# Kernel tuning notes

Measured on AMD Instinct MI355X. Metric: run time of the kernel, lower is better.

Reference implementation:

```python
import jax, jax.numpy as jnp
import numpy as np

N_NODES = 50000
N_EDGES = 800000
D = 128        # in_channels == out_channels
EDGE_DIM = 32
EPS = 0.0      # GINEConv default eps


def setup_inputs() -> dict:
    key = jax.random.key(0)
    ks = jax.random.split(key, 12)
    s = lambda d: 1.0 / np.sqrt(d)
    inp = {
        "x": jax.random.normal(ks[0], (N_NODES, D), jnp.float32),
        "edge_index": jax.random.randint(ks[1], (2, N_EDGES), 0, N_NODES, jnp.int64),
        "edge_attr": jax.random.normal(ks[2], (N_EDGES, EDGE_DIM), jnp.float32),
        "importance": jax.random.uniform(ks[3], (N_NODES, 1), jnp.float32),
        # GINEConv edge lin: Linear(edge_dim, in_channels)
        "We": jax.random.uniform(ks[4], (EDGE_DIM, D), jnp.float32, -s(EDGE_DIM), s(EDGE_DIM)),
        "be": jax.random.uniform(ks[5], (D,), jnp.float32, -s(EDGE_DIM), s(EDGE_DIM)),
        # GINEConv nn: Linear(in_channels, out_channels)
        "Wc": jax.random.uniform(ks[6], (D, D), jnp.float32, -s(D), s(D)),
        "bc": jax.random.uniform(ks[7], (D,), jnp.float32, -s(D), s(D)),
        # importance_gate: Linear(out_channels + 1, out_channels)
        "Wg": jax.random.uniform(ks[8], (D + 1, D), jnp.float32, -s(D + 1), s(D + 1)),
        "bg": jax.random.uniform(ks[9], (D,), jnp.float32, -s(D + 1), s(D + 1)),
        # importance_propagation: Linear(out_channels, 1)
        "Wp": jax.random.uniform(ks[10], (D, 1), jnp.float32, -s(D), s(D)),
        "bp": jax.random.uniform(ks[11], (1,), jnp.float32, -s(D), s(D)),
    }
    return inp


def reference(x, edge_index, edge_attr, importance, We, be, Wc, bc, Wg, bg, Wp, bp):
    src, dst = edge_index[0], edge_index[1]
    # GINEConv: messages = relu(x_j + lin(edge_attr)), aggregated by sum at dst
    e = edge_attr @ We + be                      # [E, D]
    msg = jax.nn.relu(x[src] + e)                # [E, D] gather + fused add/relu
    agg = jax.ops.segment_sum(msg, dst, num_segments=N_NODES)  # [N, D] scatter-add
    conv_out = ((1.0 + EPS) * x + agg) @ Wc + bc  # [N, D]
    # importance gating + residual
    gate_in = jnp.concatenate([conv_out, importance], axis=-1)  # [N, D+1]
    gate = jax.nn.sigmoid(gate_in @ Wg + bg)
    out = gate * conv_out + (1.0 - gate) * x
    propagated_importance = out @ Wp + bp        # [N, 1]
    return (out, propagated_importance)
```

## Files before the change

### kernel.cpp

```cpp
#include <hip/hip_runtime.h>

#define NN 50000
#define NE 800000
#define DD 128
#define ED 32
#define NB 196
#define NCH (NE / 16)

typedef short bf16x8 __attribute__((ext_vector_type(8)));
typedef float f32x4  __attribute__((ext_vector_type(4)));

__device__ __forceinline__ float4 ld4(const float* p) {
    return *reinterpret_cast<const float4*>(p);
}
__device__ __forceinline__ short f2bf(float f) {
    unsigned u = __float_as_uint(f);
    u += 0x7fffu + ((u >> 16) & 1u);
    return (short)(u >> 16);
}
__device__ __forceinline__ float bf2f(short h) {
    return __uint_as_float(((unsigned)(unsigned short)h) << 16);
}
__device__ __forceinline__ int sniff64(const int* ei) {
    return ((ei[1] | ei[3] | ei[5] | ei[7]) == 0) ? 1 : 0;
}

__global__ __launch_bounds__(256)
void k_hist(const int* __restrict__ ei, int* __restrict__ counts) {
    const int is64 = sniff64(ei);
    for (int e = blockIdx.x * blockDim.x + threadIdx.x; e < NE;
         e += gridDim.x * blockDim.x) {
        const int dst = ei[(long)(NE + e) << is64];
        atomicAdd(&counts[dst], 1);
    }
}

__global__ __launch_bounds__(256)
void k_bsum(const int* __restrict__ counts, int* __restrict__ bsum) {
    const int i = blockIdx.x * 256 + threadIdx.x;
    int c = (i < NN) ? counts[i] : 0;
#pragma unroll
    for (int off = 32; off; off >>= 1) c += __shfl_xor(c, off, 64);
    __shared__ int ws4[4];
    if ((threadIdx.x & 63) == 0) ws4[threadIdx.x >> 6] = c;
    __syncthreads();
    if (threadIdx.x == 0) bsum[blockIdx.x] = ws4[0] + ws4[1] + ws4[2] + ws4[3];
}

__global__ __launch_bounds__(256)
void k_scanb(const int* __restrict__ bsum, int* __restrict__ bexcl) {
    const int tid = threadIdx.x, lane = tid & 63, w = tid >> 6;
    const int v = (tid < NB) ? bsum[tid] : 0;
    int s = v;
#pragma unroll
    for (int off = 1; off < 64; off <<= 1) {
        const int t = __shfl_up(s, off, 64);
        if (lane >= off) s += t;
    }
    __shared__ int wsum[4], wexcl[4];
    if (lane == 63) wsum[w] = s;
    __syncthreads();
    if (tid == 0) {
        int r = 0;
#pragma unroll
        for (int k = 0; k < 4; ++k) { wexcl[k] = r; r += wsum[k]; }
    }
    __syncthreads();
    if (tid < NB) bexcl[tid] = wexcl[w] + s - v;
}

__global__ __launch_bounds__(256)
void k_rowptr(const int* __restrict__ counts, const int* __restrict__ bexcl,
              int* __restrict__ cursor) {
    const int tid = threadIdx.x, lane = tid & 63, w = tid >> 6;
    const int i = blockIdx.x * 256 + tid;
    const int c = (i < NN) ? counts[i] : 0;
    int s = c;
#pragma unroll
    for (int off = 1; off < 64; off <<= 1) {
        const int t = __shfl_up(s, off, 64);
        if (lane >= off) s += t;
    }
    __shared__ int wsum[4], wexcl[4];
    if (lane == 63) wsum[w] = s;
    __syncthreads();
    if (tid == 0) {
        int r = 0;
#pragma unroll
        for (int k = 0; k < 4; ++k) { wexcl[k] = r; r += wsum[k]; }
    }
    __syncthreads();
    if (i < NN) cursor[i] = bexcl[blockIdx.x] + wexcl[w] + s - c;
}

__global__ __launch_bounds__(256)
void k_scatter(const int* __restrict__ ei, int* __restrict__ cursor,
               int2* __restrict__ sdat, int* __restrict__ edst) {
    const int is64 = sniff64(ei);
    for (int e = blockIdx.x * blockDim.x + threadIdx.x; e < NE;
         e += gridDim.x * blockDim.x) {
        const int src = ei[(long)e << is64];
        const int dst = ei[(long)(NE + e) << is64];
        const int pos = atomicAdd(&cursor[dst], 1);
        sdat[pos] = make_int2(src, e);
        edst[pos] = dst;
    }
}

__global__ __launch_bounds__(256, 4)
void k_aggE(const float* __restrict__ x, const float* __restrict__ ea,
            const float* __restrict__ We, const float* __restrict__ be,
            const int2* __restrict__ sdat, const int* __restrict__ edst,
            float* __restrict__ agg)
{
    const int lane = threadIdx.x & 63;
    const int ncol = lane & 15;
    const int krow = (lane >> 4) << 3;
    const int grp  = lane >> 4;
    const int wid  = (blockIdx.x << 2) | (threadIdx.x >> 6);
    const int nw   = gridDim.x << 2;

    bf16x8 Bf[8];
    float beb[8];
#pragma unroll
    for (int b = 0; b < 8; ++b) {
#pragma unroll
        for (int i = 0; i < 8; ++i)
            Bf[b][i] = f2bf(We[(krow + i) * DD + b * 16 + ncol]);
        beb[b] = be[b * 16 + ncol];
    }

    if (wid >= NCH) return;

    int2 dv   = sdat[wid * 16 + ncol];
    int  dstv = edst[wid * 16 + ncol];

    for (int c = wid; c < NCH; c += nw) {
        const int cn = min(c + nw, NCH - 1);
        const int2 dvn   = sdat[cn * 16 + ncol];
        const int  dstvn = edst[cn * 16 + ncol];

        const float* ear = ea + (size_t)dv.y * ED + krow;
        const float4 r0 = ld4(ear), r1 = ld4(ear + 4);

        const float* xr[4];
#pragma unroll
        for (int r = 0; r < 4; ++r)
            xr[r] = x + (size_t)__shfl(dv.x, (grp << 2) + r, 64) * DD + ncol;
        f32x4 C[8];
#pragma unroll
        for (int b = 0; b < 8; ++b) {
            f32x4 cc;
            cc[0] = xr[0][b * 16]; cc[1] = xr[1][b * 16];
            cc[2] = xr[2][b * 16]; cc[3] = xr[3][b * 16];
            C[b] = cc;
        }

        bf16x8 Af;
        Af[0] = f2bf(r0.x); Af[1] = f2bf(r0.y);
        Af[2] = f2bf(r0.z); Af[3] = f2bf(r0.w);
        Af[4] = f2bf(r1.x); Af[5] = f2bf(r1.y);
        Af[6] = f2bf(r1.z); Af[7] = f2bf(r1.w);

#pragma unroll
        for (int b = 0; b < 8; ++b)
            C[b] = __builtin_amdgcn_mfma_f32_16x16x32_bf16(Af, Bf[b], C[b], 0, 0, 0);

        float t[8][4];
#pragma unroll
        for (int b = 0; b < 8; ++b)
#pragma unroll
            for (int r = 0; r < 4; ++r)
                t[b][r] = fmaxf(C[b][r] + beb[b], 0.0f);

        const int prv = __shfl(dstv, (lane == 0) ? 0 : lane - 1, 64);
        const bool flag = (lane < 16) && ((ncol == 0) || (dstv != prv));
        const unsigned B16 = (unsigned)__ballot(flag) & 0xFFFFu;

        int sid[4];
#pragma unroll
        for (int r = 0; r < 4; ++r) {
            const int m = (grp << 2) + r;
            sid[r] = __popc(B16 & ((2u << m) - 1)) - 1;
        }

        unsigned rem = B16;
        int s = 0;
        while (rem) {
            const int ms = __ffs((int)rem) - 1;
            rem &= rem - 1;
            const int d = __shfl(dstv, ms, 64);
            float red[8];
#pragma unroll
            for (int b = 0; b < 8; ++b) {
                float v = ((sid[0] == s) ? t[b][0] : 0.0f)
                        + ((sid[1] == s) ? t[b][1] : 0.0f)
                        + ((sid[2] == s) ? t[b][2] : 0.0f)
                        + ((sid[3] == s) ? t[b][3] : 0.0f);
                v += __shfl_xor(v, 16, 64);
                v += __shfl_xor(v, 32, 64);
                red[b] = v;
            }
            float v0 = red[0], v1 = red[4];
            v0 = (grp == 1) ? red[1] : v0;
            v0 = (grp == 2) ? red[2] : v0;
            v0 = (grp == 3) ? red[3] : v0;
            v1 = (grp == 1) ? red[5] : v1;
            v1 = (grp == 2) ? red[6] : v1;
            v1 = (grp == 3) ? red[7] : v1;
            float* ar = agg + (size_t)d * DD;
            unsafeAtomicAdd(ar + lane, v0);
            unsafeAtomicAdd(ar + 64 + lane, v1);
            ++s;
        }

        dv = dvn; dstv = dstvn;
    }
}

__global__ __launch_bounds__(256)
void k_conv(const float* __restrict__ x, const float* agg,
            const float* __restrict__ Wc, const float* __restrict__ bc,
            float* conv)
{
    __shared__ short sBh[2048 * 8];
    __shared__ short sBl[2048 * 8];
    for (int idx = threadIdx.x; idx < 2048; idx += 256) {
        const int kk = idx >> 9;
        const int b  = (idx >> 6) & 7;
        const int l  = idx & 63;
        const int row0 = kk * 32 + ((l >> 4) << 3);
        const int col  = b * 16 + (l & 15);
        bf16x8 h8, l8;
#pragma unroll
        for (int j = 0; j < 8; ++j) {
            const float v = Wc[(row0 + j) * DD + col];
            const short h = f2bf(v);
            h8[j] = h;
            l8[j] = f2bf(v - bf2f(h));
        }
        *reinterpret_cast<bf16x8*>(&sBh[idx * 8]) = h8;
        *reinterpret_cast<bf16x8*>(&sBl[idx * 8]) = l8;
    }
    __syncthreads();

    const int lane = threadIdx.x & 63;
    const int ncol = lane & 15;
    const int krow = (lane >> 4) << 3;
    const int grp  = lane >> 4;
    const int wid  = (blockIdx.x << 2) | (threadIdx.x >> 6);
    if (wid >= NN / 16) return;

    float bcb[8];
#pragma unroll
    for (int b = 0; b < 8; ++b) bcb[b] = bc[b * 16 + ncol];

    const int m0 = wid * 16;
    const float* xrow = x   + (size_t)(m0 + ncol) * DD + krow;
    const float* grow = agg + (size_t)(m0 + ncol) * DD + krow;

    f32x4 C[8];
#pragma unroll
    for (int b = 0; b < 8; ++b) {
        f32x4 c = { bcb[b], bcb[b], bcb[b], bcb[b] };
        C[b] = c;
    }

#pragma unroll
    for (int kk = 0; kk < 4; ++kk) {
        const float4 x0 = ld4(xrow + kk * 32), x1 = ld4(xrow + kk * 32 + 4);
        const float4 g0 = ld4(grow + kk * 32), g1 = ld4(grow + kk * 32 + 4);
        const float av[8] = { x0.x + g0.x, x0.y + g0.y, x0.z + g0.z, x0.w + g0.w,
                              x1.x + g1.x, x1.y + g1.y, x1.z + g1.z, x1.w + g1.w };
        bf16x8 Ah, Al;
#pragma unroll
        for (int j = 0; j < 8; ++j) {
            const short h = f2bf(av[j]);
            Ah[j] = h;
            Al[j] = f2bf(av[j] - bf2f(h));
        }
#pragma unroll
        for (int b = 0; b < 8; ++b) {
            const bf16x8 Bh = *reinterpret_cast<const bf16x8*>(&sBh[((kk * 8 + b) * 64 + lane) * 8]);
            const bf16x8 Bl = *reinterpret_cast<const bf16x8*>(&sBl[((kk * 8 + b) * 64 + lane) * 8]);
            C[b] = __builtin_amdgcn_mfma_f32_16x16x32_bf16(Ah, Bh, C[b], 0, 0, 0);
            C[b] = __builtin_amdgcn_mfma_f32_16x16x32_bf16(Al, Bh, C[b], 0, 0, 0);
            C[b] = __builtin_amdgcn_mfma_f32_16x16x32_bf16(Ah, Bl, C[b], 0, 0, 0);
        }
    }

#pragma unroll
    for (int r = 0; r < 4; ++r) {
        float* crow = conv + (size_t)(m0 + (grp << 2) + r) * DD + ncol;
#pragma unroll
        for (int b = 0; b < 8; ++b) crow[b * 16] = C[b][r];
    }
}

__global__ __launch_bounds__(256)
void k_gate(const float* __restrict__ x, const float* conv,
            const float* __restrict__ imp, const float* __restrict__ Wg,
            const float* __restrict__ bg, const float* __restrict__ Wp,
            const float* __restrict__ bp, float* outp, float* __restrict__ prop)
{
    __shared__ short sBh[2048 * 8];
    __shared__ short sBl[2048 * 8];
    for (int idx = threadIdx.x; idx < 2048; idx += 256) {
        const int kk = idx >> 9;
        const int b  = (idx >> 6) & 7;
        const int l  = idx & 63;
        const int row0 = kk * 32 + ((l >> 4) << 3);
        const int col  = b * 16 + (l & 15);
        bf16x8 h8, l8;
#pragma unroll
        for (int j = 0; j < 8; ++j) {
            const float v = Wg[(row0 + j) * DD + col];
            const short h = f2bf(v);
            h8[j] = h;
            l8[j] = f2bf(v - bf2f(h));
        }
        *reinterpret_cast<bf16x8*>(&sBh[idx * 8]) = h8;
        *reinterpret_cast<bf16x8*>(&sBl[idx * 8]) = l8;
    }
    __syncthreads();

    const int lane = threadIdx.x & 63;
    const int ncol = lane & 15;
    const int krow = (lane >> 4) << 3;
    const int grp  = lane >> 4;
    const int wid  = (blockIdx.x << 2) | (threadIdx.x >> 6);
    if (wid >= NN / 16) return;

    float bgb[8], wgi[8], wp8[8];
#pragma unroll
    for (int b = 0; b < 8; ++b) {
        bgb[b] = bg[b * 16 + ncol];
        wgi[b] = Wg[DD * DD + b * 16 + ncol];
        wp8[b] = Wp[b * 16 + ncol];
    }
    const float bps = bp[0];

    const int m0 = wid * 16;

    float cvD[8][4], xvD[8][4], im[4];
#pragma unroll
    for (int r = 0; r < 4; ++r) {
        const int m = m0 + (grp << 2) + r;
        const float* cr = conv + (size_t)m * DD + ncol;
        const float* xr = x    + (size_t)m * DD + ncol;
        im[r] = imp[m];
#pragma unroll
        for (int b = 0; b < 8; ++b) { cvD[b][r] = cr[b * 16]; xvD[b][r] = xr[b * 16]; }
    }

    f32x4 C[8];
#pragma unroll
    for (int b = 0; b < 8; ++b) {
        f32x4 c = { bgb[b], bgb[b], bgb[b], bgb[b] };
        C[b] = c;
    }

    const float* arow = conv + (size_t)(m0 + ncol) * DD + krow;
#pragma unroll
    for (int kk = 0; kk < 4; ++kk) {
        const float4 a0 = ld4(arow + kk * 32);
        const float4 a1 = ld4(arow + kk * 32 + 4);
        const float av[8] = { a0.x, a0.y, a0.z, a0.w, a1.x, a1.y, a1.z, a1.w };
        bf16x8 Ah, Al;
#pragma unroll
        for (int j = 0; j < 8; ++j) {
            const short h = f2bf(av[j]);
            Ah[j] = h;
            Al[j] = f2bf(av[j] - bf2f(h));
        }
#pragma unroll
        for (int b = 0; b < 8; ++b) {
            const bf16x8 Bh = *reinterpret_cast<const bf16x8*>(&sBh[((kk * 8 + b) * 64 + lane) * 8]);
            const bf16x8 Bl = *reinterpret_cast<const bf16x8*>(&sBl[((kk * 8 + b) * 64 + lane) * 8]);
            C[b] = __builtin_amdgcn_mfma_f32_16x16x32_bf16(Ah, Bh, C[b], 0, 0, 0);
            C[b] = __builtin_amdgcn_mfma_f32_16x16x32_bf16(Al, Bh, C[b], 0, 0, 0);
            C[b] = __builtin_amdgcn_mfma_f32_16x16x32_bf16(Ah, Bl, C[b], 0, 0, 0);
        }
    }

    float s[4] = { 0.f, 0.f, 0.f, 0.f };
#pragma unroll
    for (int r = 0; r < 4; ++r) {
        float* orow = outp + (size_t)(m0 + (grp << 2) + r) * DD + ncol;
#pragma unroll
        for (int b = 0; b < 8; ++b) {
            const float a = C[b][r] + im[r] * wgi[b];
            const float g = 1.0f / (1.0f + expf(-a));
            const float o = fmaf(g, cvD[b][r] - xvD[b][r], xvD[b][r]);
            orow[b * 16] = o;
            s[r] += o * wp8[b];
        }
    }
#pragma unroll
    for (int off = 1; off < 16; off <<= 1) {
        s[0] += __shfl_xor(s[0], off, 64);
        s[1] += __shfl_xor(s[1], off, 64);
        s[2] += __shfl_xor(s[2], off, 64);
        s[3] += __shfl_xor(s[3], off, 64);
    }
    if (ncol < 4) {
        const float v = (ncol == 0) ? s[0] : (ncol == 1) ? s[1] : (ncol == 2) ? s[2] : s[3];
        prop[m0 + (grp << 2) + ncol] = v + bps;
    }
}

extern "C" void kernel_launch(void* const* d_in, const int* in_sizes, int n_in,
                              void* d_out, int out_size, void* d_ws, size_t ws_size,
                              hipStream_t stream) {
    const float* x   = (const float*)d_in[0];
    const int*   ei  = (const int*)d_in[1];
    const float* ea  = (const float*)d_in[2];
    const float* imp = (const float*)d_in[3];
    const float* We  = (const float*)d_in[4];
    const float* be  = (const float*)d_in[5];
    const float* Wc  = (const float*)d_in[6];
    const float* bc  = (const float*)d_in[7];
    const float* Wg  = (const float*)d_in[8];
    const float* bg  = (const float*)d_in[9];
    const float* Wp  = (const float*)d_in[10];
    const float* bp  = (const float*)d_in[11];

    float* out  = (float*)d_out;
    float* prop = out + (size_t)NN * DD;
    float* agg  = out;

    int*  counts = (int*)d_ws;
    int*  cursor = (int*)((char*)d_ws + 204800);
    int*  bsum   = (int*)((char*)d_ws + 409600);
    int*  bexcl  = (int*)((char*)d_ws + 413696);
    int2* sdat   = (int2*)((char*)d_ws + 1048576);
    int*  edst   = (int*)((char*)d_ws + 7448576);

    hipMemsetAsync(counts, 0, NN * sizeof(int), stream);
    hipMemsetAsync(agg, 0, (size_t)NN * DD * sizeof(float), stream);
    hipLaunchKernelGGL(k_hist,    dim3(2048), dim3(256), 0, stream, ei, counts);
    hipLaunchKernelGGL(k_bsum,    dim3(NB),   dim3(256), 0, stream, counts, bsum);
    hipLaunchKernelGGL(k_scanb,   dim3(1),    dim3(256), 0, stream, bsum, bexcl);
    hipLaunchKernelGGL(k_rowptr,  dim3(NB),   dim3(256), 0, stream, counts, bexcl, cursor);
    hipLaunchKernelGGL(k_scatter, dim3(2048), dim3(256), 0, stream, ei, cursor, sdat, edst);
    hipLaunchKernelGGL(k_aggE,    dim3(2048), dim3(256), 0, stream,
                       x, ea, We, be, sdat, edst, agg);
    hipLaunchKernelGGL(k_conv,    dim3(782),  dim3(256), 0, stream, x, agg, Wc, bc, out);
    hipLaunchKernelGGL(k_gate,    dim3(782),  dim3(256), 0, stream,
                       x, out, imp, Wg, bg, Wp, bp, out, prop);
}
```

Baseline: 236.4 us.

## Gather bf16 copy of x and switch edge aggregation to 32x32 MFMA tiles

Adds a pre-pass that converts x to bf16 so the per-edge gather of source rows reads half the bytes. The edge kernel now processes 32-edge chunks with 32x32x16 MFMA (one chunk per wave, no persistent loop, larger grid) and replaces the segment reduction with masked FMA sums. This also rounds x to bf16 inside the message sum, which loses precision, and it drops the prefetch of the next chunk's indices. The persistent grid-stride loop that reused the We fragments is removed, so each wave reloads and converts We.

Measured after the change: 221.2 us. -6.5%, faster.

```diff
diff --git a/kernel.cpp b/kernel.cpp
--- a/kernel.cpp
+++ b/kernel.cpp
@@ -5,10 +5,12 @@
 #define DD 128
 #define ED 32
 #define NB 196
-#define NCH (NE / 16)
-
-typedef short bf16x8 __attribute__((ext_vector_type(8)));
-typedef float f32x4  __attribute__((ext_vector_type(4)));
+#define NC32 (NE / 32)
+
+typedef short  bf16x8 __attribute__((ext_vector_type(8)));
+typedef short  s16x8  __attribute__((ext_vector_type(8)));
+typedef float  f32x4  __attribute__((ext_vector_type(4)));
+typedef float  f32x16 __attribute__((ext_vector_type(16)));
 
 __device__ __forceinline__ float4 ld4(const float* p) {
     return *reinterpret_cast<const float4*>(p);
@@ -23,6 +25,17 @@
 }
 __device__ __forceinline__ int sniff64(const int* ei) {
     return ((ei[1] | ei[3] | ei[5] | ei[7]) == 0) ? 1 : 0;
+}
+
+__global__ __launch_bounds__(256)
+void k_xcast(const float* __restrict__ x, unsigned short* __restrict__ xb) {
+    const int t = blockIdx.x * 256 + threadIdx.x;
+    const int base = t * 8;
+    const float4 a = ld4(x + base), b = ld4(x + base + 4);
+    s16x8 o;
+    o[0] = f2bf(a.x); o[1] = f2bf(a.y); o[2] = f2bf(a.z); o[3] = f2bf(a.w);
+    o[4] = f2bf(b.x); o[5] = f2bf(b.y); o[6] = f2bf(b.z); o[7] = f2bf(b.w);
+    *reinterpret_cast<s16x8*>(xb + base) = o;
 }
 
 __global__ __launch_bounds__(256)
@@ -108,113 +121,96 @@
 }
 
 __global__ __launch_bounds__(256, 4)
-void k_aggE(const float* __restrict__ x, const float* __restrict__ ea,
+void k_aggE(const unsigned short* __restrict__ xb, const float* __restrict__ ea,
             const float* __restrict__ We, const float* __restrict__ be,
             const int2* __restrict__ sdat, const int* __restrict__ edst,
             float* __restrict__ agg)
 {
     const int lane = threadIdx.x & 63;
-    const int ncol = lane & 15;
-    const int krow = (lane >> 4) << 3;
-    const int grp  = lane >> 4;
+    const int col  = lane & 31;
+    const int h    = lane >> 5;
     const int wid  = (blockIdx.x << 2) | (threadIdx.x >> 6);
-    const int nw   = gridDim.x << 2;
-
-    bf16x8 Bf[8];
-    float beb[8];
-#pragma unroll
-    for (int b = 0; b < 8; ++b) {
-#pragma unroll
-        for (int i = 0; i < 8; ++i)
-            Bf[b][i] = f2bf(We[(krow + i) * DD + b * 16 + ncol]);
-        beb[b] = be[b * 16 + ncol];
-    }
-
-    if (wid >= NCH) return;
-
-    int2 dv   = sdat[wid * 16 + ncol];
-    int  dstv = edst[wid * 16 + ncol];
-
-    for (int c = wid; c < NCH; c += nw) {
-        const int cn = min(c + nw, NCH - 1);
-        const int2 dvn   = sdat[cn * 16 + ncol];
-        const int  dstvn = edst[cn * 16 + ncol];
-
-        const float* ear = ea + (size_t)dv.y * ED + krow;
-        const float4 r0 = ld4(ear), r1 = ld4(ear + 4);
-
-        const float* xr[4];
-#pragma unroll
-        for (int r = 0; r < 4; ++r)
-            xr[r] = x + (size_t)__shfl(dv.x, (grp << 2) + r, 64) * DD + ncol;
-        f32x4 C[8];
-#pragma unroll
-        for (int b = 0; b < 8; ++b) {
-            f32x4 cc;
-            cc[0] = xr[0][b * 16]; cc[1] = xr[1][b * 16];
-            cc[2] = xr[2][b * 16]; cc[3] = xr[3][b * 16];
-            C[b] = cc;
-        }
-
-        bf16x8 Af;
-        Af[0] = f2bf(r0.x); Af[1] = f2bf(r0.y);
-        Af[2] = f2bf(r0.z); Af[3] = f2bf(r0.w);
-        Af[4] = f2bf(r1.x); Af[5] = f2bf(r1.y);
-        Af[6] = f2bf(r1.z); Af[7] = f2bf(r1.w);
-
-#pragma unroll
-        for (int b = 0; b < 8; ++b)
-            C[b] = __builtin_amdgcn_mfma_f32_16x16x32_bf16(Af, Bf[b], C[b], 0, 0, 0);
-
-        float t[8][4];
-#pragma unroll
-        for (int b = 0; b < 8; ++b)
-#pragma unroll
-            for (int r = 0; r < 4; ++r)
-                t[b][r] = fmaxf(C[b][r] + beb[b], 0.0f);
-
-        const int prv = __shfl(dstv, (lane == 0) ? 0 : lane - 1, 64);
-        const bool flag = (lane < 16) && ((ncol == 0) || (dstv != prv));
-        const unsigned B16 = (unsigned)__ballot(flag) & 0xFFFFu;
-
-        int sid[4];
-#pragma unroll
-        for (int r = 0; r < 4; ++r) {
-            const int m = (grp << 2) + r;
-            sid[r] = __popc(B16 & ((2u << m) - 1)) - 1;
-        }
-
-        unsigned rem = B16;
-        int s = 0;
-        while (rem) {
-            const int ms = __ffs((int)rem) - 1;
-            rem &= rem - 1;
-            const int d = __shfl(dstv, ms, 64);
-            float red[8];
-#pragma unroll
-            for (int b = 0; b < 8; ++b) {
-                float v = ((sid[0] == s) ? t[b][0] : 0.0f)
-                        + ((sid[1] == s) ? t[b][1] : 0.0f)
-                        + ((sid[2] == s) ? t[b][2] : 0.0f)
-                        + ((sid[3] == s) ? t[b][3] : 0.0f);
-                v += __shfl_xor(v, 16, 64);
-                v += __shfl_xor(v, 32, 64);
-                red[b] = v;
-            }
-            float v0 = red[0], v1 = red[4];
-            v0 = (grp == 1) ? red[1] : v0;
-            v0 = (grp == 2) ? red[2] : v0;
-            v0 = (grp == 3) ? red[3] : v0;
-            v1 = (grp == 1) ? red[5] : v1;
-            v1 = (grp == 2) ? red[6] : v1;
-            v1 = (grp == 3) ? red[7] : v1;
-            float* ar = agg + (size_t)d * DD;
-            unsafeAtomicAdd(ar + lane, v0);
-            unsafeAtomicAdd(ar + 64 + lane, v1);
-            ++s;
-        }
-
-        dv = dvn; dstv = dstvn;
+    if (wid >= NC32) return;
+
+    bf16x8 Bf[4][2];
+    float  beb[4];
+#pragma unroll
+    for (int bb = 0; bb < 4; ++bb) {
+#pragma unroll
+        for (int s = 0; s < 2; ++s)
+#pragma unroll
+            for (int i = 0; i < 8; ++i)
+                Bf[bb][s][i] = f2bf(We[(s * 16 + h * 8 + i) * DD + bb * 32 + col]);
+        beb[bb] = be[bb * 32 + col];
+    }
+
+    const int2 dv   = sdat[wid * 32 + col];
+    const int  dstv = edst[wid * 32 + col];
+
+    unsigned off[16];
+#pragma unroll
+    for (int reg = 0; reg < 16; ++reg) {
+        const int E = (reg & 3) + 8 * (reg >> 2) + 4 * h;
+        const int src = __shfl(dv.x, E, 64);
+        off[reg] = (unsigned)src * DD + col;
+    }
+
+    f32x16 C[4];
+#pragma unroll
+    for (int bb = 0; bb < 4; ++bb)
+#pragma unroll
+        for (int reg = 0; reg < 16; ++reg)
+            C[bb][reg] = __uint_as_float((unsigned)xb[off[reg] + bb * 32] << 16);
+
+    const float* ear = ea + (size_t)dv.y * ED + h * 8;
+    const float4 a00 = ld4(ear),      a01 = ld4(ear + 4);
+    const float4 a10 = ld4(ear + 16), a11 = ld4(ear + 20);
+    bf16x8 Af0, Af1;
+    Af0[0] = f2bf(a00.x); Af0[1] = f2bf(a00.y); Af0[2] = f2bf(a00.z); Af0[3] = f2bf(a00.w);
+    Af0[4] = f2bf(a01.x); Af0[5] = f2bf(a01.y); Af0[6] = f2bf(a01.z); Af0[7] = f2bf(a01.w);
+    Af1[0] = f2bf(a10.x); Af1[1] = f2bf(a10.y); Af1[2] = f2bf(a10.z); Af1[3] = f2bf(a10.w);
+    Af1[4] = f2bf(a11.x); Af1[5] = f2bf(a11.y); Af1[6] = f2bf(a11.z); Af1[7] = f2bf(a11.w);
+
+#pragma unroll
+    for (int bb = 0; bb < 4; ++bb) {
+        C[bb] = __builtin_amdgcn_mfma_f32_32x32x16_bf16(Af0, Bf[bb][0], C[bb], 0, 0, 0);
+        C[bb] = __builtin_amdgcn_mfma_f32_32x32x16_bf16(Af1, Bf[bb][1], C[bb], 0, 0, 0);
+    }
+
+#pragma unroll
+    for (int bb = 0; bb < 4; ++bb)
+#pragma unroll
+        for (int reg = 0; reg < 16; ++reg)
+            C[bb][reg] = fmaxf(C[bb][reg] + beb[bb], 0.0f);
+
+    const int  prv  = __shfl(dstv, (col == 0) ? 0 : col - 1, 64);
+    const bool flag = (lane < 32) && ((col == 0) || (dstv != prv));
+    unsigned rem = (unsigned)(__ballot(flag) & 0xFFFFFFFFull);
+
+    while (rem) {
+        const int ms = __ffs((int)rem) - 1;
+        rem &= rem - 1;
+        const int hi = rem ? (__ffs((int)rem) - 1) : 32;
+        const int d  = __shfl(dstv, ms, 64);
+
+        float v0 = 0.f, v1 = 0.f, v2 = 0.f, v3 = 0.f;
+#pragma unroll
+        for (int reg = 0; reg < 16; ++reg) {
+            const int E = (reg & 3) + 8 * (reg >> 2) + 4 * h;
+            const float mk = (E >= ms && E < hi) ? 1.0f : 0.0f;
+            v0 = fmaf(mk, C[0][reg], v0);
+            v1 = fmaf(mk, C[1][reg], v1);
+            v2 = fmaf(mk, C[2][reg], v2);
+            v3 = fmaf(mk, C[3][reg], v3);
+        }
+        v0 += __shfl_xor(v0, 32, 64);
+        v1 += __shfl_xor(v1, 32, 64);
+        v2 += __shfl_xor(v2, 32, 64);
+        v3 += __shfl_xor(v3, 32, 64);
+
+        float* ar = agg + (size_t)d * DD + h * 64 + col;
+        unsafeAtomicAdd(ar,      h ? v2 : v0);
+        unsafeAtomicAdd(ar + 32, h ? v3 : v1);
     }
 }
 
@@ -429,22 +425,24 @@
     float* prop = out + (size_t)NN * DD;
     float* agg  = out;
 
-    int*  counts = (int*)d_ws;
-    int*  cursor = (int*)((char*)d_ws + 204800);
-    int*  bsum   = (int*)((char*)d_ws + 409600);
-    int*  bexcl  = (int*)((char*)d_ws + 413696);
-    int2* sdat   = (int2*)((char*)d_ws + 1048576);
-    int*  edst   = (int*)((char*)d_ws + 7448576);
+    int*            counts = (int*)d_ws;
+    int*            cursor = (int*)((char*)d_ws + 204800);
+    int*            bsum   = (int*)((char*)d_ws + 409600);
+    int*            bexcl  = (int*)((char*)d_ws + 413696);
+    int2*           sdat   = (int2*)((char*)d_ws + 1048576);
+    int*            edst   = (int*)((char*)d_ws + 7448576);
+    unsigned short* xb     = (unsigned short*)((char*)d_ws + 10649600);
 
     hipMemsetAsync(counts, 0, NN * sizeof(int), stream);
     hipMemsetAsync(agg, 0, (size_t)NN * DD * sizeof(float), stream);
+    hipLaunchKernelGGL(k_xcast,   dim3(3125), dim3(256), 0, stream, x, xb);
     hipLaunchKernelGGL(k_hist,    dim3(2048), dim3(256), 0, stream, ei, counts);
     hipLaunchKernelGGL(k_bsum,    dim3(NB),   dim3(256), 0, stream, counts, bsum);
     hipLaunchKernelGGL(k_scanb,   dim3(1),    dim3(256), 0, stream, bsum, bexcl);
     hipLaunchKernelGGL(k_rowptr,  dim3(NB),   dim3(256), 0, stream, counts, bexcl, cursor);
     hipLaunchKernelGGL(k_scatter, dim3(2048), dim3(256), 0, stream, ei, cursor, sdat, edst);
-    hipLaunchKernelGGL(k_aggE,    dim3(2048), dim3(256), 0, stream,
-                       x, ea, We, be, sdat, edst, agg);
+    hipLaunchKernelGGL(k_aggE,    dim3(6250), dim3(256), 0, stream,
+                       xb, ea, We, be, sdat, edst, agg);
     hipLaunchKernelGGL(k_conv,    dim3(782),  dim3(256), 0, stream, x, agg, Wc, bc, out);
     hipLaunchKernelGGL(k_gate,    dim3(782),  dim3(256), 0, stream,
                        x, out, imp, Wg, bg, Wp, bp, out, prop);
```
